# Optimization experiments

Measured on AMD Instinct MI355X. Metric: run time of the kernel, lower is better.

Reference implementation:

```python
import jax, jax.numpy as jnp
import numpy as np

N_NODES = 50000
N_EDGES = 800000
HC = 64      # hidden_channels
NG = 5       # num_gaussians
NF = 64      # num_filters
SL = 20      # short_len
NC = 2       # n_conv
Z_DIM = 2 * NF + SL  # 148
BN_EPS = 1e-5


def setup_inputs() -> dict:
    key = jax.random.key(0)
    ks = jax.random.split(key, 16)
    s = 0.05
    return {
        "h": jax.random.normal(ks[0], (N_NODES, HC), dtype=jnp.float32),
        "edge_index": jax.random.randint(ks[1], (2, N_EDGES), 0, N_NODES, dtype=jnp.int32),
        "edge_weight": jax.random.uniform(ks[2], (N_EDGES,), dtype=jnp.float32),
        "edge_attr": jax.random.uniform(ks[3], (N_EDGES, NG), dtype=jnp.float32),
        "lin0_w": jax.random.normal(ks[4], (HC, NF), dtype=jnp.float32) * s,
        "lin0_b": jnp.zeros((NF,), dtype=jnp.float32),
        "short_w": jax.random.normal(ks[5], (NG, SL), dtype=jnp.float32) * s,
        "short_b": jnp.zeros((SL,), dtype=jnp.float32),
        "linf_w": jax.random.normal(ks[6], (NC, Z_DIM, NF), dtype=jnp.float32) * s,
        "linf_b": jnp.zeros((NC, NF), dtype=jnp.float32),
        "lins_w": jax.random.normal(ks[7], (NC, Z_DIM, NF), dtype=jnp.float32) * s,
        "lins_b": jnp.zeros((NC, NF), dtype=jnp.float32),
        "bn_gamma": jnp.ones((NC, NF), dtype=jnp.float32),
        "bn_beta": jnp.zeros((NC, NF), dtype=jnp.float32),
        "data": 0,
    }


def reference(h, edge_index, edge_weight, edge_attr,
              lin0_w, lin0_b, short_w, short_b,
              linf_w, linf_b, lins_w, lins_b,
              bn_gamma, bn_beta, data):
    # lin0 + relu
    out = jax.nn.relu(h @ lin0_w + lin0_b)                      # [N, NF]
    # short edge-attr projection + relu
    ea = jax.nn.relu(edge_attr @ short_w + short_b)             # [E, SL]
    src = edge_index[0]  # x_j (source)
    dst = edge_index[1]  # x_i (target / aggregation index)
    n = out.shape[0]
    for l in range(NC):
        x_i = out[dst]                                          # [E, NF]
        x_j = out[src]                                          # [E, NF]
        z = jnp.concatenate([x_i, x_j, ea], axis=-1)            # [E, 148]
        msg = jax.nn.sigmoid(z @ linf_w[l] + linf_b[l]) * \
              jax.nn.softplus(z @ lins_w[l] + lins_b[l])        # [E, NF]
        agg = jax.ops.segment_sum(msg, dst, num_segments=n)     # [N, NF]
        # BatchNorm1d (training-mode batch stats, biased variance)
        mean = jnp.mean(agg, axis=0)
        var = jnp.mean((agg - mean) ** 2, axis=0)
        bn = (agg - mean) * jax.lax.rsqrt(var + BN_EPS) * bn_gamma[l] + bn_beta[l]
        conv_out = bn + out                                     # CGConv internal residual
        out = out + jax.nn.relu(conv_out)                       # _Interactions residual
    return out
```

## Files before the change

kernel.cpp:

```cpp
#include <hip/hip_runtime.h>
#include <hip/hip_bf16.h>

#define N_NODES 50000
#define N_EDGES 800000
#define SCAN_NB 49
#define EPW 20
#define EW_BLOCKS 10000

typedef __hip_bfloat16 bf16;
typedef unsigned int u32;
typedef unsigned short u16;
typedef _Float16 hh2 __attribute__((ext_vector_type(2)));

#if defined(__has_builtin)
#if __has_builtin(__builtin_amdgcn_fdot2)
#define HAVE_FDOT2 1
#endif
#endif

__device__ __forceinline__ float bfb(u32 b) { return __uint_as_float(b << 16); }

__device__ __forceinline__ u16 f2bf(float x) {
    bf16 a = __float2bfloat16(x);
    u16 u;
    __builtin_memcpy(&u, &a, 2);
    return u;
}

__device__ __forceinline__ hh2 pkrtz(float a, float b) {
    auto r = __builtin_amdgcn_cvt_pkrtz(a, b);
    hh2 o;
    __builtin_memcpy(&o, &r, 4);
    return o;
}

__device__ __forceinline__ float ldf(const void* p, long i, int f32) {
    if (f32) return ((const float*)p)[i];
    return bfb((u32)((const u16*)p)[i]);
}

__device__ __forceinline__ int detect_f32(const u32* g) { return g[0] == 0x3F800000u; }

__global__ __launch_bounds__(256) void k_front(const void* __restrict__ h,
        const void* __restrict__ w, const void* __restrict__ b,
        const u32* __restrict__ gr, u16* __restrict__ outw,
        const int* __restrict__ ei, int* __restrict__ cnt,
        int* __restrict__ tsum, uint4* __restrict__ aggz4) {
    int t = threadIdx.x;
    uint4 z4 = {0u, 0u, 0u, 0u};
    for (int i = blockIdx.x * 256 + t; i < N_NODES * 16; i += 1024 * 256)
        aggz4[i] = z4;
    if (blockIdx.x >= 512) {
        __shared__ int lts[SCAN_NB];
        if (t < SCAN_NB) lts[t] = 0;
        __syncthreads();
        int bid = blockIdx.x - 512;
        for (int e = bid * 256 + t; e < N_EDGES; e += 512 * 256) {
            int dst = ei[N_EDGES + e];
            atomicAdd(&cnt[dst], 1);
            atomicAdd(&lts[dst >> 10], 1);
        }
        __syncthreads();
        if (t < SCAN_NB) atomicAdd(&tsum[t], lts[t]);
        return;
    }
    __shared__ float Wl[64 * 64];
    __shared__ float bl[64];
    __shared__ float hs[16 * 64];
    int f32 = detect_f32(gr);
    for (int i = t; i < 4096; i += 256) Wl[i] = ldf(w, i, f32);
    if (t < 64) bl[t] = ldf(b, t, f32);
    int c = t & 63, g = t >> 6;
    for (int chunk = blockIdx.x; chunk < N_NODES / 16; chunk += 512) {
        __syncthreads();
        int node0 = chunk * 16;
        for (int i = t; i < 1024; i += 256) hs[i] = ldf(h, (long)node0 * 64 + i, f32);
        __syncthreads();
        #pragma unroll
        for (int nn = 0; nn < 4; ++nn) {
            int n = g * 4 + nn;
            float acc = bl[c];
            #pragma unroll
            for (int k = 0; k < 64; ++k) acc = fmaf(hs[n * 64 + k], Wl[k * 64 + c], acc);
            outw[(node0 + n) * 64 + c] = f2bf(fmaxf(acc, 0.f));
        }
    }
}

__global__ __launch_bounds__(1024) void k_scan(int* __restrict__ cnt,
        const int* __restrict__ tsum) {
    __shared__ int wsum[16];
    __shared__ int boff_s;
    int t = threadIdx.x, lane = t & 63, wv = t >> 6;
    if (wv == 0) {
        int v = (lane < SCAN_NB && lane < (int)blockIdx.x) ? tsum[lane] : 0;
        #pragma unroll
        for (int d = 32; d >= 1; d >>= 1) v += __shfl_xor(v, d, 64);
        if (lane == 0) boff_s = v;
    }
    int i = blockIdx.x * 1024 + t;
    int v = (i < N_NODES) ? cnt[i] : 0;
    int incl = v;
    #pragma unroll
    for (int d = 1; d < 64; d <<= 1) {
        int x = __shfl_up(incl, d, 64);
        if (lane >= d) incl += x;
    }
    if (lane == 63) wsum[wv] = incl;
    __syncthreads();
    if (wv == 0) {
        int s = (lane < 16) ? wsum[lane] : 0;
        int si = s;
        #pragma unroll
        for (int d = 1; d < 16; d <<= 1) {
            int x = __shfl_up(si, d, 64);
            if (lane >= d) si += x;
        }
        if (lane < 16) wsum[lane] = si - s;
    }
    __syncthreads();
    incl += wsum[wv] + boff_s;
    if (i < N_NODES) cnt[i] = incl - v;
}

__global__ __launch_bounds__(256) void k_pproj_bin(const u16* __restrict__ outw,
        const void* __restrict__ linf_w, const void* __restrict__ lins_w,
        const void* __restrict__ linf_b, const void* __restrict__ lins_b,
        const u32* __restrict__ gr, bf16* __restrict__ P,
        const int* __restrict__ ei, int* __restrict__ cursor,
        u32* __restrict__ bpack, const void* __restrict__ eattr,
        const void* __restrict__ short_w, const void* __restrict__ short_b,
        u32* __restrict__ sea, u32* __restrict__ wpk) {
    int t = threadIdx.x;
    int f32 = detect_f32(gr);
    if (blockIdx.x >= 512) {
        if (blockIdx.x == 512 && t < 128) {
            int ly = t >> 6, ln = t & 63;
            long wb = (long)ly * 9472 + 8192;
            u32* wp = wpk + (size_t)(ly * 64 + ln) * 20;
            #pragma unroll
            for (int j = 0; j < 10; ++j) {
                hh2 fp = pkrtz(ldf(linf_w, wb + (2 * j) * 64 + ln, f32),
                               ldf(linf_w, wb + (2 * j + 1) * 64 + ln, f32));
                hh2 sp = pkrtz(ldf(lins_w, wb + (2 * j) * 64 + ln, f32),
                               ldf(lins_w, wb + (2 * j + 1) * 64 + ln, f32));
                u32 uf, us;
                __builtin_memcpy(&uf, &fp, 4);
                __builtin_memcpy(&us, &sp, 4);
                wp[2 * j] = uf;
                wp[2 * j + 1] = us;
            }
        }
        __shared__ float swl[100];
        __shared__ float sbl[20];
        if (t < 100) swl[t] = ldf(short_w, t, f32);
        if (t < 20) sbl[t] = ldf(short_b, t, f32);
        __syncthreads();
        int bid = blockIdx.x - 512;
        for (int e = bid * 256 + t; e < N_EDGES; e += 512 * 256) {
            int dst = ei[N_EDGES + e];
            int src = ei[e];
            int slot = atomicAdd(&cursor[dst], 1);
            bpack[slot] = ((u32)dst << 16) | (u32)src;
            float a0 = ldf(eattr, (long)e * 5 + 0, f32);
            float a1 = ldf(eattr, (long)e * 5 + 1, f32);
            float a2 = ldf(eattr, (long)e * 5 + 2, f32);
            float a3 = ldf(eattr, (long)e * 5 + 3, f32);
            float a4 = ldf(eattr, (long)e * 5 + 4, f32);
            u32* sp = sea + (size_t)slot * 10u;
            #pragma unroll
            for (int j = 0; j < 10; ++j) {
                float e0 = sbl[2 * j], e1 = sbl[2 * j + 1];
                e0 = fmaf(a0, swl[0 * 20 + 2 * j], e0);
                e1 = fmaf(a0, swl[0 * 20 + 2 * j + 1], e1);
                e0 = fmaf(a1, swl[1 * 20 + 2 * j], e0);
                e1 = fmaf(a1, swl[1 * 20 + 2 * j + 1], e1);
                e0 = fmaf(a2, swl[2 * 20 + 2 * j], e0);
                e1 = fmaf(a2, swl[2 * 20 + 2 * j + 1], e1);
                e0 = fmaf(a3, swl[3 * 20 + 2 * j], e0);
                e1 = fmaf(a3, swl[3 * 20 + 2 * j + 1], e1);
                e0 = fmaf(a4, swl[4 * 20 + 2 * j], e0);
                e1 = fmaf(a4, swl[4 * 20 + 2 * j + 1], e1);
                e0 = fmaxf(e0, 0.f);
                e1 = fmaxf(e1, 0.f);
                hh2 h2 = pkrtz(e0, e1);
                u32 u;
                __builtin_memcpy(&u, &h2, 4);
                sp[j] = u;
            }
        }
        return;
    }
    int b = t >> 6, c = t & 63;
    const void* wmat = (b < 2) ? linf_w : lins_w;
    long woff = (long)(b & 1) * 4096;
    float bias = 0.f;
    if (b == 0) bias = ldf(linf_b, c, f32);
    if (b == 2) bias = ldf(lins_b, c, f32);
    float wc[64];
    #pragma unroll
    for (int k = 0; k < 64; ++k) wc[k] = ldf(wmat, woff + k * 64 + c, f32);
    int stidx = (b & 1) * 128 + 2 * c + (b >> 1);
    __shared__ float hs[16 * 64];
    for (int chunk = blockIdx.x; chunk < N_NODES / 16; chunk += 512) {
        __syncthreads();
        int node0 = chunk * 16;
        {
            ushort4 hv = *(const ushort4*)(outw + (size_t)node0 * 64 + t * 4);
            hs[t * 4 + 0] = bfb((u32)hv.x);
            hs[t * 4 + 1] = bfb((u32)hv.y);
            hs[t * 4 + 2] = bfb((u32)hv.z);
            hs[t * 4 + 3] = bfb((u32)hv.w);
        }
        __syncthreads();
        for (int n = 0; n < 16; ++n) {
            float acc = bias;
            #pragma unroll
            for (int k = 0; k < 64; ++k) acc = fmaf(hs[n * 64 + k], wc[k], acc);
            P[(size_t)(node0 + n) * 256 + stidx] = __float2bfloat16(acc);
        }
    }
}

struct EB { u32 ea; u32 pd[4]; u32 ps[4]; int d[4]; };

__global__ __launch_bounds__(256) void k_edge_flat(const u32* __restrict__ bpack,
        const u32* __restrict__ sea, const u32* __restrict__ wpk, int layer,
        const u32* __restrict__ Pw, float* __restrict__ agg) {
    int t = threadIdx.x, lane = t & 63, wv = t >> 6;
    int wid = blockIdx.x * 4 + wv;
    int base = wid * EPW;

    int eo = (lane / 10) & 3, j10 = lane % 10;
    const uint4* wv4 = (const uint4*)(wpk + (size_t)(layer * 64 + lane) * 20);
    uint4 q0 = wv4[0], q1 = wv4[1], q2 = wv4[2], q3 = wv4[3], q4 = wv4[4];
    u32 wbuf[20] = {q0.x, q0.y, q0.z, q0.w, q1.x, q1.y, q1.z, q1.w,
                    q2.x, q2.y, q2.z, q2.w, q3.x, q3.y, q3.z, q3.w,
                    q4.x, q4.y, q4.z, q4.w};
    hh2 wf2[10], ws2[10];
    #pragma unroll
    for (int j = 0; j < 10; ++j) {
        __builtin_memcpy(&wf2[j], &wbuf[2 * j], 4);
        __builtin_memcpy(&ws2[j], &wbuf[2 * j + 1], 4);
    }

    float acc = 0.f;
    int cur = -1;

    auto issueA = [&](u32& Apk, int b) {
        Apk = bpack[(u32)base + 4u * (u32)b + ((u32)lane & 3u)];
    };
    auto issueB = [&](EB& B, u32 Apk, int b) {
        B.ea = sea[(u32)(base + 4 * b + eo) * 10u + (u32)j10];
        #pragma unroll
        for (int i = 0; i < 4; ++i) {
            u32 pki = (u32)__builtin_amdgcn_readlane((int)Apk, i);
            int d = (int)(pki >> 16);
            u32 s = pki & 0xFFFFu;
            B.d[i] = d;
            B.pd[i] = Pw[(u32)d * 128u + (u32)lane];
            B.ps[i] = Pw[s * 128u + 64u + (u32)lane];
        }
    };
    auto computeC = [&](const EB& B) {
        #pragma unroll
        for (int i = 0; i < 4; ++i) {
            int d = B.d[i];
            u32 pd = B.pd[i], ps = B.ps[i];
            float f = bfb(pd & 0xFFFFu) + bfb(ps & 0xFFFFu);
            float s = __uint_as_float(pd & 0xFFFF0000u) +
                      __uint_as_float(ps & 0xFFFF0000u);
            #pragma unroll
            for (int j = 0; j < 10; ++j) {
                u32 u = (u32)__builtin_amdgcn_readlane((int)B.ea, 10 * i + j);
                hh2 hu;
                __builtin_memcpy(&hu, &u, 4);
#ifdef HAVE_FDOT2
                f = __builtin_amdgcn_fdot2(hu, wf2[j], f, false);
                s = __builtin_amdgcn_fdot2(hu, ws2[j], s, false);
#else
                f = fmaf((float)hu[0], (float)wf2[j][0], f);
                f = fmaf((float)hu[1], (float)wf2[j][1], f);
                s = fmaf((float)hu[0], (float)ws2[j][0], s);
                s = fmaf((float)hu[1], (float)ws2[j][1], s);
#endif
            }
            float sig = 1.f / (1.f + __expf(-f));
            float sp = fmaxf(s, 0.f) + __logf(1.f + __expf(-fabsf(s)));
            if (d != cur) {
                if (cur >= 0)
                    atomicAdd(agg + (u32)cur * 64u + (u32)lane, acc);
                acc = 0.f;
                cur = d;
            }
            acc += sig * sp;
        }
    };

    u32 A0, A1, A2, A3;
    EB B0, B1, B2, B3;
    issueA(A0, 0); issueA(A1, 1); issueA(A2, 2); issueA(A3, 3);
    issueB(B0, A0, 0); issueB(B1, A1, 1); issueB(B2, A2, 2);
    issueA(A0, 4);
    issueB(B3, A3, 3);
    computeC(B0);
    issueB(B0, A0, 4);
    computeC(B1);
    computeC(B2);
    computeC(B3);
    computeC(B0);
    if (cur >= 0) atomicAdd(agg + (u32)cur * 64u + (u32)lane, acc);
}

__global__ __launch_bounds__(256) void k_stats(const float* __restrict__ aggf,
        float* __restrict__ stats) {
    int t = threadIdx.x;
    int r = t >> 4, c4 = (t & 15) * 4;
    float s0 = 0.f, s1 = 0.f, s2 = 0.f, s3 = 0.f;
    float q0 = 0.f, q1 = 0.f, q2 = 0.f, q3 = 0.f;
    for (int row = blockIdx.x * 16 + r; row < N_NODES; row += 256 * 16) {
        float4 v = *(const float4*)(aggf + (size_t)row * 64 + c4);
        s0 += v.x; s1 += v.y; s2 += v.z; s3 += v.w;
        q0 = fmaf(v.x, v.x, q0); q1 = fmaf(v.y, v.y, q1);
        q2 = fmaf(v.z, v.z, q2); q3 = fmaf(v.w, v.w, q3);
    }
    __shared__ float red[2][16][64];
    red[0][r][c4 + 0] = s0; red[0][r][c4 + 1] = s1;
    red[0][r][c4 + 2] = s2; red[0][r][c4 + 3] = s3;
    red[1][r][c4 + 0] = q0; red[1][r][c4 + 1] = q1;
    red[1][r][c4 + 2] = q2; red[1][r][c4 + 3] = q3;
    __syncthreads();
    if (t < 128) {
        int m = t >> 6, c = t & 63;
        float a = 0.f;
        #pragma unroll
        for (int k = 0; k < 16; ++k) a += red[m][k][c];
        atomicAdd(&stats[m * 64 + c], a);
    }
}

__global__ __launch_bounds__(256) void k_apply_pproj(float* __restrict__ aggf,
        const float* __restrict__ stats, const void* __restrict__ gamma,
        const void* __restrict__ beta, const u32* __restrict__ gr,
        u16* __restrict__ outw,
        const void* __restrict__ linf_w, const void* __restrict__ lins_w,
        const void* __restrict__ linf_b, const void* __restrict__ lins_b,
        bf16* __restrict__ P) {
    int f32 = detect_f32(gr);
    int t = threadIdx.x;
    int b = t >> 6, c = t & 63;
    int nid = t >> 4, c4 = (t & 15) * 4;
    const float invN = 1.f / (float)N_NODES;
    float m4[4], iv4[4], g4[4], b4[4];
    #pragma unroll
    for (int k = 0; k < 4; ++k) {
        float mean = stats[c4 + k] * invN;
        float var = fmaxf(stats[64 + c4 + k] * invN - mean * mean, 0.f);
        m4[k] = mean;
        iv4[k] = rsqrtf(var + 1e-5f);
        g4[k] = ldf(gamma, c4 + k, f32);
        b4[k] = ldf(beta, c4 + k, f32);
    }
    const void* wmat = (b < 2) ? linf_w : lins_w;
    long woff = 9472 + (long)(b & 1) * 4096;
    float bias = 0.f;
    if (b == 0) bias = ldf(linf_b, 64 + c, f32);
    if (b == 2) bias = ldf(lins_b, 64 + c, f32);
    float wc[64];
    #pragma unroll
    for (int k = 0; k < 64; ++k) wc[k] = ldf(wmat, woff + k * 64 + c, f32);
    int stidx = (b & 1) * 128 + 2 * c + (b >> 1);
    __shared__ float hs[16 * 64];
    for (int chunk = blockIdx.x; chunk < N_NODES / 16; chunk += 512) {
        __syncthreads();
        int node0 = chunk * 16;
        {
            size_t idx = (size_t)(node0 + nid) * 64 + c4;
            float4 a = *(const float4*)(aggf + idx);
            ushort4 ow = *(const ushort4*)(outw + idx);
            const float* ap = (const float*)&a;
            const u16* op = (const u16*)&ow;
            float no[4];
            #pragma unroll
            for (int k = 0; k < 4; ++k) {
                float o = bfb((u32)op[k]);
                float bn = fmaf((ap[k] - m4[k]) * iv4[k], g4[k], b4[k]);
                no[k] = o + fmaxf(bn + o, 0.f);
            }
            ushort4 nw = {f2bf(no[0]), f2bf(no[1]), f2bf(no[2]), f2bf(no[3])};
            *(ushort4*)(outw + idx) = nw;
            float4 z4 = {0.f, 0.f, 0.f, 0.f};
            *(float4*)(aggf + idx) = z4;
            float4 hv = {no[0], no[1], no[2], no[3]};
            *(float4*)(&hs[nid * 64 + c4]) = hv;
        }
        __syncthreads();
        for (int n = 0; n < 16; ++n) {
            float acc = bias;
            #pragma unroll
            for (int k = 0; k < 64; ++k) acc = fmaf(hs[n * 64 + k], wc[k], acc);
            P[(size_t)(node0 + n) * 256 + stidx] = __float2bfloat16(acc);
        }
    }
}

__global__ __launch_bounds__(256) void k_apply_final(const float* __restrict__ aggf,
        const float* __restrict__ stats, const void* __restrict__ gamma,
        const void* __restrict__ beta, const u32* __restrict__ gr,
        const u16* __restrict__ outw, void* __restrict__ dout) {
    int f32 = detect_f32(gr);
    const float invN = 1.f / (float)N_NODES;
    int t0 = blockIdx.x * 256 + threadIdx.x;
    int c4 = (t0 & 15) * 4;
    float m4[4], iv4[4], g4[4], b4[4];
    #pragma unroll
    for (int k = 0; k < 4; ++k) {
        float mean = stats[c4 + k] * invN;
        float var = fmaxf(stats[64 + c4 + k] * invN - mean * mean, 0.f);
        m4[k] = mean;
        iv4[k] = rsqrtf(var + 1e-5f);
        g4[k] = ldf(gamma, 64 + c4 + k, f32);
        b4[k] = ldf(beta, 64 + c4 + k, f32);
    }
    for (int i4 = t0; i4 < N_NODES * 16; i4 += 1024 * 256) {
        float4 a = *(const float4*)(aggf + (size_t)i4 * 4);
        ushort4 ow = *(const ushort4*)(outw + (size_t)i4 * 4);
        const float* ap = (const float*)&a;
        const u16* op = (const u16*)&ow;
        float no[4];
        #pragma unroll
        for (int k = 0; k < 4; ++k) {
            float o = bfb((u32)op[k]);
            float bn = fmaf((ap[k] - m4[k]) * iv4[k], g4[k], b4[k]);
            no[k] = o + fmaxf(bn + o, 0.f);
        }
        if (f32) {
            float4 o4 = {no[0], no[1], no[2], no[3]};
            *(float4*)((float*)dout + (size_t)i4 * 4) = o4;
        } else {
            ushort4 o4 = {f2bf(no[0]), f2bf(no[1]), f2bf(no[2]), f2bf(no[3])};
            *(ushort4*)((u16*)dout + (size_t)i4 * 4) = o4;
        }
    }
}

extern "C" void kernel_launch(void* const* d_in, const int* in_sizes, int n_in,
                              void* d_out, int out_size, void* d_ws, size_t ws_size,
                              hipStream_t stream) {
    const void* h       = d_in[0];
    const int*  ei      = (const int*)d_in[1];
    const void* eattr   = d_in[3];
    const void* lin0_w  = d_in[4];
    const void* lin0_b  = d_in[5];
    const void* short_w = d_in[6];
    const void* short_b = d_in[7];
    const void* linf_w  = d_in[8];
    const void* linf_b  = d_in[9];
    const void* lins_w  = d_in[10];
    const void* lins_b  = d_in[11];
    const void* gamma   = d_in[12];
    const void* beta    = d_in[13];
    const u32*  gr      = (const u32*)gamma;

    u16*   outw  = (u16*)d_ws;
    bf16*  P     = (bf16*)(outw + (size_t)N_NODES * 64);
    u32*   bpack = (u32*)(P + (size_t)N_NODES * 256);
    float* aggf  = (float*)(bpack + N_EDGES);
    int*   cnt   = (int*)(aggf + (size_t)N_NODES * 64);
    float* stats = (float*)(cnt + N_NODES);
    int*   tsum  = (int*)(stats + 256);
    u32*   sea   = (u32*)(tsum + 64);
    u32*   wpk   = sea + (size_t)N_EDGES * 10;

    size_t zbytes = (size_t)N_NODES * 4 + 256 * 4 + 64 * 4;
    (void)hipMemsetAsync(cnt, 0, zbytes, stream);

    k_front<<<1024, 256, 0, stream>>>(h, lin0_w, lin0_b, gr, outw, ei, cnt,
                                      tsum, (uint4*)aggf);
    k_scan<<<SCAN_NB, 1024, 0, stream>>>(cnt, tsum);
    k_pproj_bin<<<1024, 256, 0, stream>>>(outw, linf_w, lins_w, linf_b, lins_b,
                                          gr, P, ei, cnt, bpack, eattr,
                                          short_w, short_b, sea, wpk);
    k_edge_flat<<<EW_BLOCKS, 256, 0, stream>>>(bpack, sea, wpk, 0,
                                               (const u32*)P, aggf);
    k_stats<<<256, 256, 0, stream>>>(aggf, stats);
    k_apply_pproj<<<512, 256, 0, stream>>>(aggf, stats, gamma, beta, gr, outw,
                                           linf_w, lins_w, linf_b, lins_b, P);
    k_edge_flat<<<EW_BLOCKS, 256, 0, stream>>>(bpack, sea, wpk, 1,
                                               (const u32*)P, aggf);
    k_stats<<<256, 256, 0, stream>>>(aggf, stats + 128);
    k_apply_final<<<1024, 256, 0, stream>>>(aggf, stats + 128, gamma, beta, gr,
                                            outw, d_out);
}
```

Measured before the change: 442.3 us.

## Split edge-attr projection into separate kernel reading in sorted slot order

Binning now records the original edge id next to the packed dst/src pair. The short edge-attr projection moves out of the binning blocks into a new kernel that walks slots in order, gathers edge_attr by the stored id, and writes sea with coalesced 8-byte stores instead of scattered 40-byte rows. The binning and node-projection work are also spread over all 1024 blocks instead of being split 512/512. In exchange this adds a kernel launch, random gathers of edge_attr, and a doubled bin array whose strided reads in the edge kernel use half of each fetched line.

Measured after the change: 477.7 us. 1.08x slower.

```diff
diff --git a/kernel.cpp b/kernel.cpp
--- a/kernel.cpp
+++ b/kernel.cpp
@@ -128,68 +128,34 @@
         const void* __restrict__ linf_b, const void* __restrict__ lins_b,
         const u32* __restrict__ gr, bf16* __restrict__ P,
         const int* __restrict__ ei, int* __restrict__ cursor,
-        u32* __restrict__ bpack, const void* __restrict__ eattr,
-        const void* __restrict__ short_w, const void* __restrict__ short_b,
-        u32* __restrict__ sea, u32* __restrict__ wpk) {
+        uint2* __restrict__ bb, u32* __restrict__ wpk) {
     int t = threadIdx.x;
     int f32 = detect_f32(gr);
-    if (blockIdx.x >= 512) {
-        if (blockIdx.x == 512 && t < 128) {
-            int ly = t >> 6, ln = t & 63;
-            long wb = (long)ly * 9472 + 8192;
-            u32* wp = wpk + (size_t)(ly * 64 + ln) * 20;
-            #pragma unroll
-            for (int j = 0; j < 10; ++j) {
-                hh2 fp = pkrtz(ldf(linf_w, wb + (2 * j) * 64 + ln, f32),
-                               ldf(linf_w, wb + (2 * j + 1) * 64 + ln, f32));
-                hh2 sp = pkrtz(ldf(lins_w, wb + (2 * j) * 64 + ln, f32),
-                               ldf(lins_w, wb + (2 * j + 1) * 64 + ln, f32));
-                u32 uf, us;
-                __builtin_memcpy(&uf, &fp, 4);
-                __builtin_memcpy(&us, &sp, 4);
-                wp[2 * j] = uf;
-                wp[2 * j + 1] = us;
-            }
-        }
-        __shared__ float swl[100];
-        __shared__ float sbl[20];
-        if (t < 100) swl[t] = ldf(short_w, t, f32);
-        if (t < 20) sbl[t] = ldf(short_b, t, f32);
-        __syncthreads();
-        int bid = blockIdx.x - 512;
-        for (int e = bid * 256 + t; e < N_EDGES; e += 512 * 256) {
-            int dst = ei[N_EDGES + e];
-            int src = ei[e];
-            int slot = atomicAdd(&cursor[dst], 1);
-            bpack[slot] = ((u32)dst << 16) | (u32)src;
-            float a0 = ldf(eattr, (long)e * 5 + 0, f32);
-            float a1 = ldf(eattr, (long)e * 5 + 1, f32);
-            float a2 = ldf(eattr, (long)e * 5 + 2, f32);
-            float a3 = ldf(eattr, (long)e * 5 + 3, f32);
-            float a4 = ldf(eattr, (long)e * 5 + 4, f32);
-            u32* sp = sea + (size_t)slot * 10u;
-            #pragma unroll
-            for (int j = 0; j < 10; ++j) {
-                float e0 = sbl[2 * j], e1 = sbl[2 * j + 1];
-                e0 = fmaf(a0, swl[0 * 20 + 2 * j], e0);
-                e1 = fmaf(a0, swl[0 * 20 + 2 * j + 1], e1);
-                e0 = fmaf(a1, swl[1 * 20 + 2 * j], e0);
-                e1 = fmaf(a1, swl[1 * 20 + 2 * j + 1], e1);
-                e0 = fmaf(a2, swl[2 * 20 + 2 * j], e0);
-                e1 = fmaf(a2, swl[2 * 20 + 2 * j + 1], e1);
-                e0 = fmaf(a3, swl[3 * 20 + 2 * j], e0);
-                e1 = fmaf(a3, swl[3 * 20 + 2 * j + 1], e1);
-                e0 = fmaf(a4, swl[4 * 20 + 2 * j], e0);
-                e1 = fmaf(a4, swl[4 * 20 + 2 * j + 1], e1);
-                e0 = fmaxf(e0, 0.f);
-                e1 = fmaxf(e1, 0.f);
-                hh2 h2 = pkrtz(e0, e1);
-                u32 u;
-                __builtin_memcpy(&u, &h2, 4);
-                sp[j] = u;
-            }
-        }
-        return;
+    if (blockIdx.x == 0 && t < 128) {
+        int ly = t >> 6, ln = t & 63;
+        long wb = (long)ly * 9472 + 8192;
+        u32* wp = wpk + (size_t)(ly * 64 + ln) * 20;
+        #pragma unroll
+        for (int j = 0; j < 10; ++j) {
+            hh2 fp = pkrtz(ldf(linf_w, wb + (2 * j) * 64 + ln, f32),
+                           ldf(linf_w, wb + (2 * j + 1) * 64 + ln, f32));
+            hh2 sp = pkrtz(ldf(lins_w, wb + (2 * j) * 64 + ln, f32),
+                           ldf(lins_w, wb + (2 * j + 1) * 64 + ln, f32));
+            u32 uf, us;
+            __builtin_memcpy(&uf, &fp, 4);
+            __builtin_memcpy(&us, &sp, 4);
+            wp[2 * j] = uf;
+            wp[2 * j + 1] = us;
+        }
+    }
+    for (int e = blockIdx.x * 256 + t; e < N_EDGES; e += 1024 * 256) {
+        int dst = ei[N_EDGES + e];
+        int src = ei[e];
+        int slot = atomicAdd(&cursor[dst], 1);
+        uint2 v;
+        v.x = ((u32)dst << 16) | (u32)src;
+        v.y = (u32)e;
+        bb[slot] = v;
     }
     int b = t >> 6, c = t & 63;
     const void* wmat = (b < 2) ? linf_w : lins_w;
@@ -202,7 +168,7 @@
     for (int k = 0; k < 64; ++k) wc[k] = ldf(wmat, woff + k * 64 + c, f32);
     int stidx = (b & 1) * 128 + 2 * c + (b >> 1);
     __shared__ float hs[16 * 64];
-    for (int chunk = blockIdx.x; chunk < N_NODES / 16; chunk += 512) {
+    for (int chunk = blockIdx.x; chunk < N_NODES / 16; chunk += 1024) {
         __syncthreads();
         int node0 = chunk * 16;
         {
@@ -222,9 +188,56 @@
     }
 }
 
+__global__ __launch_bounds__(256) void k_sea(const uint2* __restrict__ bb,
+        const void* __restrict__ eattr, const void* __restrict__ short_w,
+        const void* __restrict__ short_b, const u32* __restrict__ gr,
+        u32* __restrict__ sea) {
+    __shared__ float swl[100];
+    __shared__ float sbl[20];
+    int t = threadIdx.x;
+    int f32 = detect_f32(gr);
+    if (t < 100) swl[t] = ldf(short_w, t, f32);
+    if (t < 20) sbl[t] = ldf(short_b, t, f32);
+    __syncthreads();
+    int slot = blockIdx.x * 256 + t;
+    u32 eid = bb[slot].y;
+    float a0 = ldf(eattr, (long)eid * 5 + 0, f32);
+    float a1 = ldf(eattr, (long)eid * 5 + 1, f32);
+    float a2 = ldf(eattr, (long)eid * 5 + 2, f32);
+    float a3 = ldf(eattr, (long)eid * 5 + 3, f32);
+    float a4 = ldf(eattr, (long)eid * 5 + 4, f32);
+    u32 buf[10];
+    #pragma unroll
+    for (int j = 0; j < 10; ++j) {
+        float e0 = sbl[2 * j], e1 = sbl[2 * j + 1];
+        e0 = fmaf(a0, swl[0 * 20 + 2 * j], e0);
+        e1 = fmaf(a0, swl[0 * 20 + 2 * j + 1], e1);
+        e0 = fmaf(a1, swl[1 * 20 + 2 * j], e0);
+        e1 = fmaf(a1, swl[1 * 20 + 2 * j + 1], e1);
+        e0 = fmaf(a2, swl[2 * 20 + 2 * j], e0);
+        e1 = fmaf(a2, swl[2 * 20 + 2 * j + 1], e1);
+        e0 = fmaf(a3, swl[3 * 20 + 2 * j], e0);
+        e1 = fmaf(a3, swl[3 * 20 + 2 * j + 1], e1);
+        e0 = fmaf(a4, swl[4 * 20 + 2 * j], e0);
+        e1 = fmaf(a4, swl[4 * 20 + 2 * j + 1], e1);
+        e0 = fmaxf(e0, 0.f);
+        e1 = fmaxf(e1, 0.f);
+        hh2 h2 = pkrtz(e0, e1);
+        u32 u;
+        __builtin_memcpy(&u, &h2, 4);
+        buf[j] = u;
+    }
+    u32* sp = sea + (size_t)slot * 10u;
+    #pragma unroll
+    for (int q = 0; q < 5; ++q) {
+        uint2 v2 = {buf[2 * q], buf[2 * q + 1]};
+        *(uint2*)(sp + 2 * q) = v2;
+    }
+}
+
 struct EB { u32 ea; u32 pd[4]; u32 ps[4]; int d[4]; };
 
-__global__ __launch_bounds__(256) void k_edge_flat(const u32* __restrict__ bpack,
+__global__ __launch_bounds__(256) void k_edge_flat(const u32* __restrict__ bbu,
         const u32* __restrict__ sea, const u32* __restrict__ wpk, int layer,
         const u32* __restrict__ Pw, float* __restrict__ agg) {
     int t = threadIdx.x, lane = t & 63, wv = t >> 6;
@@ -248,7 +261,7 @@
     int cur = -1;
 
     auto issueA = [&](u32& Apk, int b) {
-        Apk = bpack[(u32)base + 4u * (u32)b + ((u32)lane & 3u)];
+        Apk = bbu[2u * ((u32)base + 4u * (u32)b + ((u32)lane & 3u))];
     };
     auto issueB = [&](EB& B, u32 Apk, int b) {
         B.ea = sea[(u32)(base + 4 * b + eo) * 10u + (u32)j10];
@@ -464,8 +477,8 @@
 
     u16*   outw  = (u16*)d_ws;
     bf16*  P     = (bf16*)(outw + (size_t)N_NODES * 64);
-    u32*   bpack = (u32*)(P + (size_t)N_NODES * 256);
-    float* aggf  = (float*)(bpack + N_EDGES);
+    uint2* bb    = (uint2*)(P + (size_t)N_NODES * 256);
+    float* aggf  = (float*)(bb + N_EDGES);
     int*   cnt   = (int*)(aggf + (size_t)N_NODES * 64);
     float* stats = (float*)(cnt + N_NODES);
     int*   tsum  = (int*)(stats + 256);
@@ -479,14 +492,14 @@
                                       tsum, (uint4*)aggf);
     k_scan<<<SCAN_NB, 1024, 0, stream>>>(cnt, tsum);
     k_pproj_bin<<<1024, 256, 0, stream>>>(outw, linf_w, lins_w, linf_b, lins_b,
-                                          gr, P, ei, cnt, bpack, eattr,
-                                          short_w, short_b, sea, wpk);
-    k_edge_flat<<<EW_BLOCKS, 256, 0, stream>>>(bpack, sea, wpk, 0,
+                                          gr, P, ei, cnt, bb, wpk);
+    k_sea<<<N_EDGES / 256, 256, 0, stream>>>(bb, eattr, short_w, short_b, gr, sea);
+    k_edge_flat<<<EW_BLOCKS, 256, 0, stream>>>((const u32*)bb, sea, wpk, 0,
                                                (const u32*)P, aggf);
     k_stats<<<256, 256, 0, stream>>>(aggf, stats);
     k_apply_pproj<<<512, 256, 0, stream>>>(aggf, stats, gamma, beta, gr, outw,
                                            linf_w, lins_w, linf_b, lins_b, P);
-    k_edge_flat<<<EW_BLOCKS, 256, 0, stream>>>(bpack, sea, wpk, 1,
+    k_edge_flat<<<EW_BLOCKS, 256, 0, stream>>>((const u32*)bb, sea, wpk, 1,
                                                (const u32*)P, aggf);
     k_stats<<<256, 256, 0, stream>>>(aggf, stats + 128);
     k_apply_final<<<1024, 256, 0, stream>>>(aggf, stats + 128, gamma, beta, gr,
```

## Compute edge-attr projection in edge order and gather it via stored edge ids

Applied to the files above, without the earlier changes.

The short edge-attribute projection moves from the binning kernel into the front kernel as an extra block range. It writes results in original edge order with coalesced 8-byte stores, instead of scattering them to sorted slots. The bin array becomes uint2 so each entry also holds the original edge id. The edge kernel reads that id through a shuffle and gathers the projected attributes indirectly. This takes the scattered 40-byte writes off the critical binning pass, but makes the per-edge attribute reads in both edge layers non-contiguous and doubles the size of the bin array.

New measurement: 459.7 us. 3.9% more time.

```diff
diff --git a/kernel.cpp b/kernel.cpp
--- a/kernel.cpp
+++ b/kernel.cpp
@@ -45,129 +45,28 @@
         const void* __restrict__ w, const void* __restrict__ b,
         const u32* __restrict__ gr, u16* __restrict__ outw,
         const int* __restrict__ ei, int* __restrict__ cnt,
-        int* __restrict__ tsum, uint4* __restrict__ aggz4) {
+        int* __restrict__ tsum, uint4* __restrict__ aggz4,
+        const void* __restrict__ eattr, const void* __restrict__ short_w,
+        const void* __restrict__ short_b, u32* __restrict__ sea_e) {
     int t = threadIdx.x;
     uint4 z4 = {0u, 0u, 0u, 0u};
-    for (int i = blockIdx.x * 256 + t; i < N_NODES * 16; i += 1024 * 256)
+    for (int i = blockIdx.x * 256 + t; i < N_NODES * 16; i += 1536 * 256)
         aggz4[i] = z4;
-    if (blockIdx.x >= 512) {
-        __shared__ int lts[SCAN_NB];
-        if (t < SCAN_NB) lts[t] = 0;
-        __syncthreads();
-        int bid = blockIdx.x - 512;
-        for (int e = bid * 256 + t; e < N_EDGES; e += 512 * 256) {
-            int dst = ei[N_EDGES + e];
-            atomicAdd(&cnt[dst], 1);
-            atomicAdd(&lts[dst >> 10], 1);
-        }
-        __syncthreads();
-        if (t < SCAN_NB) atomicAdd(&tsum[t], lts[t]);
-        return;
-    }
-    __shared__ float Wl[64 * 64];
-    __shared__ float bl[64];
-    __shared__ float hs[16 * 64];
     int f32 = detect_f32(gr);
-    for (int i = t; i < 4096; i += 256) Wl[i] = ldf(w, i, f32);
-    if (t < 64) bl[t] = ldf(b, t, f32);
-    int c = t & 63, g = t >> 6;
-    for (int chunk = blockIdx.x; chunk < N_NODES / 16; chunk += 512) {
-        __syncthreads();
-        int node0 = chunk * 16;
-        for (int i = t; i < 1024; i += 256) hs[i] = ldf(h, (long)node0 * 64 + i, f32);
-        __syncthreads();
-        #pragma unroll
-        for (int nn = 0; nn < 4; ++nn) {
-            int n = g * 4 + nn;
-            float acc = bl[c];
-            #pragma unroll
-            for (int k = 0; k < 64; ++k) acc = fmaf(hs[n * 64 + k], Wl[k * 64 + c], acc);
-            outw[(node0 + n) * 64 + c] = f2bf(fmaxf(acc, 0.f));
-        }
-    }
-}
-
-__global__ __launch_bounds__(1024) void k_scan(int* __restrict__ cnt,
-        const int* __restrict__ tsum) {
-    __shared__ int wsum[16];
-    __shared__ int boff_s;
-    int t = threadIdx.x, lane = t & 63, wv = t >> 6;
-    if (wv == 0) {
-        int v = (lane < SCAN_NB && lane < (int)blockIdx.x) ? tsum[lane] : 0;
-        #pragma unroll
-        for (int d = 32; d >= 1; d >>= 1) v += __shfl_xor(v, d, 64);
-        if (lane == 0) boff_s = v;
-    }
-    int i = blockIdx.x * 1024 + t;
-    int v = (i < N_NODES) ? cnt[i] : 0;
-    int incl = v;
-    #pragma unroll
-    for (int d = 1; d < 64; d <<= 1) {
-        int x = __shfl_up(incl, d, 64);
-        if (lane >= d) incl += x;
-    }
-    if (lane == 63) wsum[wv] = incl;
-    __syncthreads();
-    if (wv == 0) {
-        int s = (lane < 16) ? wsum[lane] : 0;
-        int si = s;
-        #pragma unroll
-        for (int d = 1; d < 16; d <<= 1) {
-            int x = __shfl_up(si, d, 64);
-            if (lane >= d) si += x;
-        }
-        if (lane < 16) wsum[lane] = si - s;
-    }
-    __syncthreads();
-    incl += wsum[wv] + boff_s;
-    if (i < N_NODES) cnt[i] = incl - v;
-}
-
-__global__ __launch_bounds__(256) void k_pproj_bin(const u16* __restrict__ outw,
-        const void* __restrict__ linf_w, const void* __restrict__ lins_w,
-        const void* __restrict__ linf_b, const void* __restrict__ lins_b,
-        const u32* __restrict__ gr, bf16* __restrict__ P,
-        const int* __restrict__ ei, int* __restrict__ cursor,
-        u32* __restrict__ bpack, const void* __restrict__ eattr,
-        const void* __restrict__ short_w, const void* __restrict__ short_b,
-        u32* __restrict__ sea, u32* __restrict__ wpk) {
-    int t = threadIdx.x;
-    int f32 = detect_f32(gr);
-    if (blockIdx.x >= 512) {
-        if (blockIdx.x == 512 && t < 128) {
-            int ly = t >> 6, ln = t & 63;
-            long wb = (long)ly * 9472 + 8192;
-            u32* wp = wpk + (size_t)(ly * 64 + ln) * 20;
-            #pragma unroll
-            for (int j = 0; j < 10; ++j) {
-                hh2 fp = pkrtz(ldf(linf_w, wb + (2 * j) * 64 + ln, f32),
-                               ldf(linf_w, wb + (2 * j + 1) * 64 + ln, f32));
-                hh2 sp = pkrtz(ldf(lins_w, wb + (2 * j) * 64 + ln, f32),
-                               ldf(lins_w, wb + (2 * j + 1) * 64 + ln, f32));
-                u32 uf, us;
-                __builtin_memcpy(&uf, &fp, 4);
-                __builtin_memcpy(&us, &sp, 4);
-                wp[2 * j] = uf;
-                wp[2 * j + 1] = us;
-            }
-        }
+    if (blockIdx.x >= 1024) {
         __shared__ float swl[100];
         __shared__ float sbl[20];
         if (t < 100) swl[t] = ldf(short_w, t, f32);
         if (t < 20) sbl[t] = ldf(short_b, t, f32);
         __syncthreads();
-        int bid = blockIdx.x - 512;
+        int bid = blockIdx.x - 1024;
         for (int e = bid * 256 + t; e < N_EDGES; e += 512 * 256) {
-            int dst = ei[N_EDGES + e];
-            int src = ei[e];
-            int slot = atomicAdd(&cursor[dst], 1);
-            bpack[slot] = ((u32)dst << 16) | (u32)src;
             float a0 = ldf(eattr, (long)e * 5 + 0, f32);
             float a1 = ldf(eattr, (long)e * 5 + 1, f32);
             float a2 = ldf(eattr, (long)e * 5 + 2, f32);
             float a3 = ldf(eattr, (long)e * 5 + 3, f32);
             float a4 = ldf(eattr, (long)e * 5 + 4, f32);
-            u32* sp = sea + (size_t)slot * 10u;
+            u32 buf[10];
             #pragma unroll
             for (int j = 0; j < 10; ++j) {
                 float e0 = sbl[2 * j], e1 = sbl[2 * j + 1];
@@ -186,8 +85,124 @@
                 hh2 h2 = pkrtz(e0, e1);
                 u32 u;
                 __builtin_memcpy(&u, &h2, 4);
-                sp[j] = u;
+                buf[j] = u;
             }
+            u32* sp = sea_e + (size_t)e * 10u;
+            #pragma unroll
+            for (int q = 0; q < 5; ++q) {
+                uint2 v2 = {buf[2 * q], buf[2 * q + 1]};
+                *(uint2*)(sp + 2 * q) = v2;
+            }
+        }
+        return;
+    }
+    if (blockIdx.x >= 512) {
+        __shared__ int lts[SCAN_NB];
+        if (t < SCAN_NB) lts[t] = 0;
+        __syncthreads();
+        int bid = blockIdx.x - 512;
+        for (int e = bid * 256 + t; e < N_EDGES; e += 512 * 256) {
+            int dst = ei[N_EDGES + e];
+            atomicAdd(&cnt[dst], 1);
+            atomicAdd(&lts[dst >> 10], 1);
+        }
+        __syncthreads();
+        if (t < SCAN_NB) atomicAdd(&tsum[t], lts[t]);
+        return;
+    }
+    __shared__ float Wl[64 * 64];
+    __shared__ float bl[64];
+    __shared__ float hs[16 * 64];
+    for (int i = t; i < 4096; i += 256) Wl[i] = ldf(w, i, f32);
+    if (t < 64) bl[t] = ldf(b, t, f32);
+    int c = t & 63, g = t >> 6;
+    for (int chunk = blockIdx.x; chunk < N_NODES / 16; chunk += 512) {
+        __syncthreads();
+        int node0 = chunk * 16;
+        for (int i = t; i < 1024; i += 256) hs[i] = ldf(h, (long)node0 * 64 + i, f32);
+        __syncthreads();
+        #pragma unroll
+        for (int nn = 0; nn < 4; ++nn) {
+            int n = g * 4 + nn;
+            float acc = bl[c];
+            #pragma unroll
+            for (int k = 0; k < 64; ++k) acc = fmaf(hs[n * 64 + k], Wl[k * 64 + c], acc);
+            outw[(node0 + n) * 64 + c] = f2bf(fmaxf(acc, 0.f));
+        }
+    }
+}
+
+__global__ __launch_bounds__(1024) void k_scan(int* __restrict__ cnt,
+        const int* __restrict__ tsum) {
+    __shared__ int wsum[16];
+    __shared__ int boff_s;
+    int t = threadIdx.x, lane = t & 63, wv = t >> 6;
+    if (wv == 0) {
+        int v = (lane < SCAN_NB && lane < (int)blockIdx.x) ? tsum[lane] : 0;
+        #pragma unroll
+        for (int d = 32; d >= 1; d >>= 1) v += __shfl_xor(v, d, 64);
+        if (lane == 0) boff_s = v;
+    }
+    int i = blockIdx.x * 1024 + t;
+    int v = (i < N_NODES) ? cnt[i] : 0;
+    int incl = v;
+    #pragma unroll
+    for (int d = 1; d < 64; d <<= 1) {
+        int x = __shfl_up(incl, d, 64);
+        if (lane >= d) incl += x;
+    }
+    if (lane == 63) wsum[wv] = incl;
+    __syncthreads();
+    if (wv == 0) {
+        int s = (lane < 16) ? wsum[lane] : 0;
+        int si = s;
+        #pragma unroll
+        for (int d = 1; d < 16; d <<= 1) {
+            int x = __shfl_up(si, d, 64);
+            if (lane >= d) si += x;
+        }
+        if (lane < 16) wsum[lane] = si - s;
+    }
+    __syncthreads();
+    incl += wsum[wv] + boff_s;
+    if (i < N_NODES) cnt[i] = incl - v;
+}
+
+__global__ __launch_bounds__(256) void k_pproj_bin(const u16* __restrict__ outw,
+        const void* __restrict__ linf_w, const void* __restrict__ lins_w,
+        const void* __restrict__ linf_b, const void* __restrict__ lins_b,
+        const u32* __restrict__ gr, bf16* __restrict__ P,
+        const int* __restrict__ ei, int* __restrict__ cursor,
+        uint2* __restrict__ bb, u32* __restrict__ wpk) {
+    int t = threadIdx.x;
+    int f32 = detect_f32(gr);
+    if (blockIdx.x >= 512) {
+        if (blockIdx.x == 512 && t < 128) {
+            int ly = t >> 6, ln = t & 63;
+            long wb = (long)ly * 9472 + 8192;
+            u32* wp = wpk + (size_t)(ly * 64 + ln) * 20;
+            #pragma unroll
+            for (int j = 0; j < 10; ++j) {
+                hh2 fp = pkrtz(ldf(linf_w, wb + (2 * j) * 64 + ln, f32),
+                               ldf(linf_w, wb + (2 * j + 1) * 64 + ln, f32));
+                hh2 sp = pkrtz(ldf(lins_w, wb + (2 * j) * 64 + ln, f32),
+                               ldf(lins_w, wb + (2 * j + 1) * 64 + ln, f32));
+                u32 uf, us;
+                __builtin_memcpy(&uf, &fp, 4);
+                __builtin_memcpy(&us, &sp, 4);
+                wp[2 * j] = uf;
+                wp[2 * j + 1] = us;
+            }
+        }
+        int bid = blockIdx.x - 512;
+        for (int e = bid * 256 + t; e < N_EDGES; e += 512 * 256) {
+            int dst = ei[N_EDGES + e];
+            int src = ei[e];
+            int slot = atomicAdd(&cursor[dst], 1);
+            uint2 v;
+            v.x = ((u32)dst << 16) | (u32)src;
+            v.y = (u32)e;
+            bb[slot] = v;
         }
         return;
     }
@@ -224,8 +239,8 @@
 
 struct EB { u32 ea; u32 pd[4]; u32 ps[4]; int d[4]; };
 
-__global__ __launch_bounds__(256) void k_edge_flat(const u32* __restrict__ bpack,
-        const u32* __restrict__ sea, const u32* __restrict__ wpk, int layer,
+__global__ __launch_bounds__(256) void k_edge_flat(const uint2* __restrict__ bb,
+        const u32* __restrict__ sea_e, const u32* __restrict__ wpk, int layer,
         const u32* __restrict__ Pw, float* __restrict__ agg) {
     int t = threadIdx.x, lane = t & 63, wv = t >> 6;
     int wid = blockIdx.x * 4 + wv;
@@ -247,14 +262,15 @@
     float acc = 0.f;
     int cur = -1;
 
-    auto issueA = [&](u32& Apk, int b) {
-        Apk = bpack[(u32)base + 4u * (u32)b + ((u32)lane & 3u)];
+    auto issueA = [&](uint2& A, int b) {
+        A = bb[(u32)base + 4u * (u32)b + ((u32)lane & 3u)];
     };
-    auto issueB = [&](EB& B, u32 Apk, int b) {
-        B.ea = sea[(u32)(base + 4 * b + eo) * 10u + (u32)j10];
+    auto issueB = [&](EB& B, uint2 A, int b) {
+        u32 eid = (u32)__shfl((int)A.y, eo, 64);
+        B.ea = sea_e[eid * 10u + (u32)j10];
         #pragma unroll
         for (int i = 0; i < 4; ++i) {
-            u32 pki = (u32)__builtin_amdgcn_readlane((int)Apk, i);
+            u32 pki = (u32)__builtin_amdgcn_readlane((int)A.x, i);
             int d = (int)(pki >> 16);
             u32 s = pki & 0xFFFFu;
             B.d[i] = d;
@@ -297,7 +313,7 @@
         }
     };
 
-    u32 A0, A1, A2, A3;
+    uint2 A0, A1, A2, A3;
     EB B0, B1, B2, B3;
     issueA(A0, 0); issueA(A1, 1); issueA(A2, 2); issueA(A3, 3);
     issueB(B0, A0, 0); issueB(B1, A1, 1); issueB(B2, A2, 2);
@@ -464,29 +480,29 @@
 
     u16*   outw  = (u16*)d_ws;
     bf16*  P     = (bf16*)(outw + (size_t)N_NODES * 64);
-    u32*   bpack = (u32*)(P + (size_t)N_NODES * 256);
-    float* aggf  = (float*)(bpack + N_EDGES);
+    uint2* bb    = (uint2*)(P + (size_t)N_NODES * 256);
+    float* aggf  = (float*)(bb + N_EDGES);
     int*   cnt   = (int*)(aggf + (size_t)N_NODES * 64);
     float* stats = (float*)(cnt + N_NODES);
     int*   tsum  = (int*)(stats + 256);
-    u32*   sea   = (u32*)(tsum + 64);
-    u32*   wpk   = sea + (size_t)N_EDGES * 10;
+    u32*   sea_e = (u32*)(tsum + 64);
+    u32*   wpk   = sea_e + (size_t)N_EDGES * 10;
 
     size_t zbytes = (size_t)N_NODES * 4 + 256 * 4 + 64 * 4;
     (void)hipMemsetAsync(cnt, 0, zbytes, stream);
 
-    k_front<<<1024, 256, 0, stream>>>(h, lin0_w, lin0_b, gr, outw, ei, cnt,
-                                      tsum, (uint4*)aggf);
+    k_front<<<1536, 256, 0, stream>>>(h, lin0_w, lin0_b, gr, outw, ei, cnt,
+                                      tsum, (uint4*)aggf, eattr, short_w,
+                                      short_b, sea_e);
     k_scan<<<SCAN_NB, 1024, 0, stream>>>(cnt, tsum);
     k_pproj_bin<<<1024, 256, 0, stream>>>(outw, linf_w, lins_w, linf_b, lins_b,
-                                          gr, P, ei, cnt, bpack, eattr,
-                                          short_w, short_b, sea, wpk);
-    k_edge_flat<<<EW_BLOCKS, 256, 0, stream>>>(bpack, sea, wpk, 0,
+                                          gr, P, ei, cnt, bb, wpk);
+    k_edge_flat<<<EW_BLOCKS, 256, 0, stream>>>(bb, sea_e, wpk, 0,
                                                (const u32*)P, aggf);
     k_stats<<<256, 256, 0, stream>>>(aggf, stats);
     k_apply_pproj<<<512, 256, 0, stream>>>(aggf, stats, gamma, beta, gr, outw,
                                            linf_w, lins_w, linf_b, lins_b, P);
-    k_edge_flat<<<EW_BLOCKS, 256, 0, stream>>>(bpack, sea, wpk, 1,
+    k_edge_flat<<<EW_BLOCKS, 256, 0, stream>>>(bb, sea_e, wpk, 1,
                                                (const u32*)P, aggf);
     k_stats<<<256, 256, 0, stream>>>(aggf, stats + 128);
     k_apply_final<<<1024, 256, 0, stream>>>(aggf, stats + 128, gamma, beta, gr,
```
